# Optimization experiments

Measured on AMD Instinct MI355X. Metric: run time of the kernel, lower is better.

Reference implementation:

```python
import jax, jax.numpy as jnp
import numpy as np

D = 256       # d_model
NH = 8        # heads
K = 7         # neighborhood kernel size
DFF = 1024    # feedforward dim
EPS = 1e-5
B, H, W = 4, 56, 56


def layer_norm(x, g, b):
    m = jnp.mean(x, axis=-1, keepdims=True)
    v = jnp.mean((x - m) ** 2, axis=-1, keepdims=True)
    return (x - m) * jax.lax.rsqrt(v + EPS) * g + b


def neighborhood_attn(x, W_qkv, b_qkv, W_proj, b_proj):
    # NATTEN NeighborhoodAttention2D: each query attends to a KxK window
    # centered on it, clamped (shifted) at borders so every query sees K*K keys.
    Bx, Hx, Wx, C = x.shape
    hd = C // NH
    qkv = x @ W_qkv + b_qkv                      # [B,H,W,3C]
    q, k, v = jnp.split(qkv, 3, axis=-1)
    q = q.reshape(Bx, Hx, Wx, NH, hd)
    k = k.reshape(Bx, Hx, Wx, NH, hd)
    v = v.reshape(Bx, Hx, Wx, NH, hd)
    # neighbor index grids: start = clip(i - K//2, 0, H-K), window = start + [0..K)
    ih = jnp.clip(jnp.arange(Hx) - K // 2, 0, Hx - K)[:, None] + jnp.arange(K)  # [H,K]
    iw = jnp.clip(jnp.arange(Wx) - K // 2, 0, Wx - K)[:, None] + jnp.arange(K)  # [W,K]
    # gather K/V neighborhoods -> [B,H,W,K,K,NH,hd]
    k_nb = k[:, ih[:, None, :, None], iw[None, :, None, :]]
    v_nb = v[:, ih[:, None, :, None], iw[None, :, None, :]]
    attn = jnp.einsum('bhwnd,bhwijnd->bhwnij', q, k_nb) * (hd ** -0.5)
    attn = jax.nn.softmax(attn.reshape(Bx, Hx, Wx, NH, K * K), axis=-1)
    attn = attn.reshape(Bx, Hx, Wx, NH, K, K)
    out = jnp.einsum('bhwnij,bhwijnd->bhwnd', attn, v_nb).reshape(Bx, Hx, Wx, C)
    return out @ W_proj + b_proj


def setup_inputs() -> dict:
    key = jax.random.key(0)
    ks = jax.random.split(key, 8)
    s = 0.02
    return {
        'x': jax.random.normal(ks[0], (B, H, W, D), dtype=jnp.float32),
        'W_qkv': jax.random.normal(ks[1], (D, 3 * D), dtype=jnp.float32) * s,
        'b_qkv': jnp.zeros((3 * D,), dtype=jnp.float32),
        'W_proj': jax.random.normal(ks[2], (D, D), dtype=jnp.float32) * s,
        'b_proj': jnp.zeros((D,), dtype=jnp.float32),
        'W1': jax.random.normal(ks[3], (D, DFF), dtype=jnp.float32) * s,
        'b1': jnp.zeros((DFF,), dtype=jnp.float32),
        'W2': jax.random.normal(ks[4], (DFF, D), dtype=jnp.float32) * s,
        'b2': jnp.zeros((D,), dtype=jnp.float32),
        'g1': jnp.ones((D,), dtype=jnp.float32),
        'be1': jnp.zeros((D,), dtype=jnp.float32),
        'g2': jnp.ones((D,), dtype=jnp.float32),
        'be2': jnp.zeros((D,), dtype=jnp.float32),
    }


def reference(x, W_qkv, b_qkv, W_proj, b_proj, W1, b1, W2, b2, g1, be1, g2, be2):
    # norm_first=False (post-norm): x = norm1(x + mha(x)); x = norm2(x + ff(x))
    a = neighborhood_attn(x, W_qkv, b_qkv, W_proj, b_proj)
    x = layer_norm(x + a, g1, be1)
    f = jax.nn.relu(x @ W1 + b1) @ W2 + b2
    return layer_norm(x + f, g2, be2)
```

## Files before the change

### kernel.cpp

```cpp
#include <hip/hip_runtime.h>
#include <math.h>

#define BATCH 4
#define HH 56
#define WW 56
#define DMODEL 256
#define NHEADS 8
#define HD 32
#define NNB 49
#define NTOK (BATCH*HH*WW)

#define HALO 22
#define NHTOK (HALO*HALO)
#define KV_PAD 40

typedef __attribute__((ext_vector_type(8))) short s16x8;
typedef __attribute__((ext_vector_type(4))) float f32x4;
typedef __attribute__((ext_vector_type(2))) float f32x2;

__device__ inline unsigned short f2b(float f) {
    union { float f; unsigned int u; } v; v.f = f;
    unsigned int r = v.u + 0x7FFF + ((v.u >> 16) & 1);
    return (unsigned short)(r >> 16);
}
__device__ inline float b2f(unsigned short u) {
    union { float f; unsigned int u; } v; v.u = ((unsigned int)u) << 16;
    return v.f;
}

__device__ __forceinline__ f32x2 unpk(unsigned int u) {
    union { unsigned int u; float f; } lo, hi;
    lo.u = u << 16;
    hi.u = u & 0xffff0000u;
    return f32x2{lo.f, hi.f};
}

__device__ __forceinline__ f32x2 pk_fma(f32x2 a, f32x2 b, f32x2 c) {
#if __has_builtin(__builtin_elementwise_fma)
    return __builtin_elementwise_fma(a, b, c);
#else
    return f32x2{fmaf(a.x, b.x, c.x), fmaf(a.y, b.y, c.y)};
#endif
}

__device__ __forceinline__ void async16(const unsigned short* g, unsigned short* l) {
    __builtin_amdgcn_global_load_lds(
        (const __attribute__((address_space(1))) unsigned int*)g,
        (__attribute__((address_space(3))) unsigned int*)l, 16, 0, 0);
}

#define XCAST_BLOCKS 1568
__global__ __launch_bounds__(256)
void prep_kernel(const float* __restrict__ x,
                 const float* __restrict__ Wq, const float* __restrict__ Wp,
                 const float* __restrict__ W1, const float* __restrict__ W2,
                 unsigned short* __restrict__ xb,
                 unsigned short* __restrict__ Wqb, unsigned short* __restrict__ Wpb,
                 unsigned short* __restrict__ W1b, unsigned short* __restrict__ W2b)
{
    if (blockIdx.x < XCAST_BLOCKS) {
        const int i = blockIdx.x * 256 + threadIdx.x;
        const float4* xp = (const float4*)x + (size_t)i * 2;
        const float4 a = xp[0], b = xp[1];
        s16x8 o;
        o[0] = (short)f2b(a.x); o[1] = (short)f2b(a.y);
        o[2] = (short)f2b(a.z); o[3] = (short)f2b(a.w);
        o[4] = (short)f2b(b.x); o[5] = (short)f2b(b.y);
        o[6] = (short)f2b(b.z); o[7] = (short)f2b(b.w);
        *((s16x8*)xb + i) = o;
        return;
    }
    int i = (blockIdx.x - XCAST_BLOCKS) * 256 + threadIdx.x;
    if (i < 196608) {
        int n = i >> 8, k = i & 255;
        Wqb[i] = f2b(Wq[k * 768 + n]);
    } else if ((i -= 196608) < 65536) {
        int n = i >> 8, k = i & 255;
        Wpb[i] = f2b(Wp[k * 256 + n]);
    } else if ((i -= 65536) < 262144) {
        int n = i >> 8, k = i & 255;
        W1b[i] = f2b(W1[k * 1024 + n]);
    } else {
        i -= 262144;
        int n = i >> 10, k = i & 1023;
        W2b[i] = f2b(W2[k * 256 + n]);
    }
}

template<int BN, bool AF32>
__global__ __launch_bounds__(256)
void gemm_k(const unsigned short* __restrict__ Ab, const float* __restrict__ Af,
            const unsigned short* __restrict__ Bt, const float* __restrict__ bias,
            float* __restrict__ outf, unsigned short* __restrict__ outb,
            int M, int N, int K, int relu)
{
    constexpr int NB  = BN / 32;
    constexpr int BPW = BN / 32;
    __shared__ unsigned short As[128 * 64];
    __shared__ unsigned short Bs[BN * 64];

    const int tid = threadIdx.x;
    const int bm = blockIdx.y * 128, bn = blockIdx.x * BN;
    const int wid = tid >> 6, lane = tid & 63;
    const int wm = (wid >> 1) * 64, wn = (wid & 1) * (BN / 2);
    const int row16 = lane & 15, quad = lane >> 4;
    const int crow = lane >> 3, ck8 = (lane & 7) * 8;

    f32x4 acc[4][NB] = {};

    for (int k0 = 0; k0 < K; k0 += 64) {
        float4 fv[8];
        if (AF32) {
            const float* g = Af + (size_t)(bm + (tid >> 1)) * K + k0 + (tid & 1) * 32;
            #pragma unroll
            for (int u = 0; u < 8; ++u) fv[u] = *(const float4*)(g + u * 4);
        }
        __syncthreads();
        if (AF32) {
            unsigned short* d = As + (tid >> 1) * 64 + (tid & 1) * 32;
            #pragma unroll
            for (int u = 0; u < 4; ++u) {
                s16x8 o;
                o[0] = (short)f2b(fv[2*u].x);   o[1] = (short)f2b(fv[2*u].y);
                o[2] = (short)f2b(fv[2*u].z);   o[3] = (short)f2b(fv[2*u].w);
                o[4] = (short)f2b(fv[2*u+1].x); o[5] = (short)f2b(fv[2*u+1].y);
                o[6] = (short)f2b(fv[2*u+1].z); o[7] = (short)f2b(fv[2*u+1].w);
                *(s16x8*)(d + u * 8) = o;
            }
        } else {
            #pragma unroll
            for (int c = 0; c < 4; ++c) {
                const int ch = wid * 4 + c;
                async16(Ab + (size_t)(bm + ch * 8 + crow) * K + k0 + ck8, As + ch * 512);
            }
        }
        #pragma unroll
        for (int c = 0; c < BPW; ++c) {
            const int ch = wid * BPW + c;
            async16(Bt + (size_t)(bn + ch * 8 + crow) * K + k0 + ck8, Bs + ch * 512);
        }
        __syncthreads();

        #pragma unroll
        for (int kc = 0; kc < 2; ++kc) {
            s16x8 af[4], bf[NB];
            #pragma unroll
            for (int i = 0; i < 4; ++i)
                af[i] = *(const s16x8*)(As + (wm + i * 16 + row16) * 64 + kc * 32 + quad * 8);
            #pragma unroll
            for (int j = 0; j < NB; ++j)
                bf[j] = *(const s16x8*)(Bs + (wn + j * 16 + row16) * 64 + kc * 32 + quad * 8);
            #pragma unroll
            for (int i = 0; i < 4; ++i)
                #pragma unroll
                for (int j = 0; j < NB; ++j)
                    acc[i][j] = __builtin_amdgcn_mfma_f32_16x16x32_bf16(af[i], bf[j], acc[i][j], 0, 0, 0);
        }
    }

    #pragma unroll
    for (int j = 0; j < NB; ++j) {
        const int col = bn + wn + j * 16 + row16;
        const float bb = bias[col];
        #pragma unroll
        for (int i = 0; i < 4; ++i) {
            const int r0 = bm + wm + i * 16 + quad * 4;
            #pragma unroll
            for (int reg = 0; reg < 4; ++reg) {
                float v = acc[i][j][reg] + bb;
                if (relu) v = fmaxf(v, 0.f);
                if (outf) outf[(size_t)(r0 + reg) * N + col] = v;
                if (outb) outb[(size_t)(r0 + reg) * N + col] = f2b(v);
            }
        }
    }
}

__global__ __launch_bounds__(256)
void gemm_ln(const unsigned short* __restrict__ Ab, const unsigned short* __restrict__ Bt,
             const float* __restrict__ bias, const float* __restrict__ resid,
             const float* __restrict__ g, const float* __restrict__ beta,
             float* __restrict__ outf, unsigned short* __restrict__ outb, int K)
{
    __shared__ unsigned short As[32 * 64];
    __shared__ unsigned short Bs[256 * 64];

    const int tid = threadIdx.x;
    const int bm = blockIdx.x * 32;
    const int wid = tid >> 6, lane = tid & 63;
    const int wn = wid * 64;
    const int row16 = lane & 15, quad = lane >> 4;
    const int crow = lane >> 3, ck8 = (lane & 7) * 8;

    f32x4 acc[2][4] = {};

    for (int k0 = 0; k0 < K; k0 += 64) {
        __syncthreads();
        #pragma unroll
        for (int c = 0; c < 9; ++c) {
            const int ch = wid * 9 + c;
            if (ch < 4) {
                async16(Ab + (size_t)(bm + ch * 8 + crow) * K + k0 + ck8, As + ch * 512);
            } else {
                const int bc = ch - 4;
                async16(Bt + (size_t)(bc * 8 + crow) * K + k0 + ck8, Bs + bc * 512);
            }
        }
        __syncthreads();

        #pragma unroll
        for (int kc = 0; kc < 2; ++kc) {
            s16x8 af[2], bf[4];
            #pragma unroll
            for (int i = 0; i < 2; ++i)
                af[i] = *(const s16x8*)(As + (i * 16 + row16) * 64 + kc * 32 + quad * 8);
            #pragma unroll
            for (int j = 0; j < 4; ++j)
                bf[j] = *(const s16x8*)(Bs + (wn + j * 16 + row16) * 64 + kc * 32 + quad * 8);
            #pragma unroll
            for (int i = 0; i < 2; ++i)
                #pragma unroll
                for (int j = 0; j < 4; ++j)
                    acc[i][j] = __builtin_amdgcn_mfma_f32_16x16x32_bf16(af[i], bf[j], acc[i][j], 0, 0, 0);
        }
    }

    float bb[4], gv[4], bev[4];
    #pragma unroll
    for (int j = 0; j < 4; ++j) {
        const int col = wn + j * 16 + row16;
        bb[j] = bias[col]; gv[j] = g[col]; bev[j] = beta[col];
    }
    #pragma unroll
    for (int i = 0; i < 2; ++i) {
        #pragma unroll
        for (int reg = 0; reg < 4; ++reg) {
            const size_t rb = (size_t)(bm + i * 16 + quad * 4 + reg) * 256;
            #pragma unroll
            for (int j = 0; j < 4; ++j)
                acc[i][j][reg] += bb[j] + resid[rb + wn + j * 16 + row16];
        }
    }

    __syncthreads();
    float* red = (float*)As;
    #pragma unroll
    for (int i = 0; i < 2; ++i) {
        #pragma unroll
        for (int reg = 0; reg < 4; ++reg) {
            float s1 = 0.f, s2 = 0.f;
            #pragma unroll
            for (int j = 0; j < 4; ++j) {
                const float t = acc[i][j][reg];
                s1 += t; s2 += t * t;
            }
            #pragma unroll
            for (int o = 1; o < 16; o <<= 1) {
                s1 += __shfl_xor(s1, o, 64);
                s2 += __shfl_xor(s2, o, 64);
            }
            if (row16 == 0) {
                const int lrow = i * 16 + quad * 4 + reg;
                red[lrow * 8 + wid * 2]     = s1;
                red[lrow * 8 + wid * 2 + 1] = s2;
            }
        }
    }
    __syncthreads();
    float* stats = red + 256;
    if (tid < 32) {
        const float S1 = red[tid*8] + red[tid*8+2] + red[tid*8+4] + red[tid*8+6];
        const float S2 = red[tid*8+1] + red[tid*8+3] + red[tid*8+5] + red[tid*8+7];
        const float m = S1 * (1.0f / 256.0f);
        const float var = S2 * (1.0f / 256.0f) - m * m;
        stats[tid * 2]     = m;
        stats[tid * 2 + 1] = rsqrtf(var + 1e-5f);
    }
    __syncthreads();

    #pragma unroll
    for (int i = 0; i < 2; ++i) {
        #pragma unroll
        for (int reg = 0; reg < 4; ++reg) {
            const int lrow = i * 16 + quad * 4 + reg;
            const float m = stats[lrow * 2], r = stats[lrow * 2 + 1];
            const size_t rb = (size_t)(bm + lrow) * 256;
            #pragma unroll
            for (int j = 0; j < 4; ++j) {
                const int col = wn + j * 16 + row16;
                const float o = (acc[i][j][reg] - m) * r * gv[j] + bev[j];
                outf[rb + col] = o;
                if (outb) outb[rb + col] = f2b(o);
            }
        }
    }
}

__global__ __launch_bounds__(256, 2)
void natt_kernel(const unsigned short* __restrict__ qkvb, unsigned short* __restrict__ att)
{
    const int blk  = blockIdx.x;
    const int head = blk & 7;
    const int t2   = blk >> 3;
    const int tile = t2 & 15;
    const int b    = t2 >> 4;
    const int r0 = (tile >> 2) * 16, c0 = (tile & 3) * 16;
    const int hs = min(max(r0 - 3, 0), 34);
    const int ws = min(max(c0 - 3, 0), 34);

    __shared__ unsigned short Ks[NHTOK * KV_PAD];
    __shared__ unsigned short Vs[NHTOK * KV_PAD];

    const int tid = threadIdx.x;

    #pragma unroll
    for (int it = 0; it < 8; ++it) {
        const int t = it * 64 + (tid >> 2);
        if (t < NHTOK) {
            const int hr = t / HALO, hc = t - hr * HALO;
            const size_t rb = ((size_t)((b * 56 + hs + hr) * 56 + (ws + hc))) * 768;
            const int d8 = (tid & 3) * 8;
            *(s16x8*)(Ks + t * KV_PAD + d8) = *(const s16x8*)(qkvb + rb + 256 + head * 32 + d8);
            *(s16x8*)(Vs + t * KV_PAD + d8) = *(const s16x8*)(qkvb + rb + 512 + head * 32 + d8);
        }
    }

    const int qh = min(r0 + (tid >> 4), 55);
    const int qw = min(c0 + (tid & 15), 55);
    const int tok = (b * 56 + qh) * 56 + qw;
    const int ro = min(max(qh - 3, 0), 49) - hs;
    const int co = min(max(qw - 3, 0), 49) - ws;

    f32x2 qf[16];
    {
        const unsigned int* qp = (const unsigned int*)(qkvb + (size_t)tok * 768 + head * 32);
        #pragma unroll
        for (int p = 0; p < 16; ++p)
            qf[p] = unpk(qp[p]) * 0.17677669529663687f;
    }
    __syncthreads();

    f32x2 acc[16] = {};
    float sum = 0.f;
    for (int i = 0; i < 7; ++i) {
        const int trow = (ro + i) * HALO + co;
        #pragma unroll
        for (int j = 0; j < 7; ++j) {
            const unsigned int* kp = (const unsigned int*)(Ks + (trow + j) * KV_PAD);
            const unsigned int* vp = (const unsigned int*)(Vs + (trow + j) * KV_PAD);
            const uint4 ka = *(const uint4*)(kp);
            const uint4 kb = *(const uint4*)(kp + 4);
            const uint4 kc = *(const uint4*)(kp + 8);
            const uint4 kd = *(const uint4*)(kp + 12);
            const uint4 va = *(const uint4*)(vp);
            const uint4 vb = *(const uint4*)(vp + 4);
            const uint4 vc = *(const uint4*)(vp + 8);
            const uint4 vd = *(const uint4*)(vp + 12);
            f32x2 sa = {0.f, 0.f}, sb = {0.f, 0.f};
            sa = pk_fma(qf[0],  unpk(ka.x), sa);  sb = pk_fma(qf[1],  unpk(ka.y), sb);
            sa = pk_fma(qf[2],  unpk(ka.z), sa);  sb = pk_fma(qf[3],  unpk(ka.w), sb);
            sa = pk_fma(qf[4],  unpk(kb.x), sa);  sb = pk_fma(qf[5],  unpk(kb.y), sb);
            sa = pk_fma(qf[6],  unpk(kb.z), sa);  sb = pk_fma(qf[7],  unpk(kb.w), sb);
            sa = pk_fma(qf[8],  unpk(kc.x), sa);  sb = pk_fma(qf[9],  unpk(kc.y), sb);
            sa = pk_fma(qf[10], unpk(kc.z), sa);  sb = pk_fma(qf[11], unpk(kc.w), sb);
            sa = pk_fma(qf[12], unpk(kd.x), sa);  sb = pk_fma(qf[13], unpk(kd.y), sb);
            sa = pk_fma(qf[14], unpk(kd.z), sa);  sb = pk_fma(qf[15], unpk(kd.w), sb);
            const float p = __expf(sa.x + sa.y + sb.x + sb.y);
            sum += p;
            const f32x2 pv = {p, p};
            acc[0]  = pk_fma(pv, unpk(va.x), acc[0]);
            acc[1]  = pk_fma(pv, unpk(va.y), acc[1]);
            acc[2]  = pk_fma(pv, unpk(va.z), acc[2]);
            acc[3]  = pk_fma(pv, unpk(va.w), acc[3]);
            acc[4]  = pk_fma(pv, unpk(vb.x), acc[4]);
            acc[5]  = pk_fma(pv, unpk(vb.y), acc[5]);
            acc[6]  = pk_fma(pv, unpk(vb.z), acc[6]);
            acc[7]  = pk_fma(pv, unpk(vb.w), acc[7]);
            acc[8]  = pk_fma(pv, unpk(vc.x), acc[8]);
            acc[9]  = pk_fma(pv, unpk(vc.y), acc[9]);
            acc[10] = pk_fma(pv, unpk(vc.z), acc[10]);
            acc[11] = pk_fma(pv, unpk(vc.w), acc[11]);
            acc[12] = pk_fma(pv, unpk(vd.x), acc[12]);
            acc[13] = pk_fma(pv, unpk(vd.y), acc[13]);
            acc[14] = pk_fma(pv, unpk(vd.z), acc[14]);
            acc[15] = pk_fma(pv, unpk(vd.w), acc[15]);
        }
    }
    const float inv = 1.0f / sum;

    unsigned short* op = att + (size_t)tok * DMODEL + head * 32;
    #pragma unroll
    for (int d4 = 0; d4 < 8; ++d4) {
        ushort4 o;
        o.x = f2b(acc[d4 * 2].x     * inv);
        o.y = f2b(acc[d4 * 2].y     * inv);
        o.z = f2b(acc[d4 * 2 + 1].x * inv);
        o.w = f2b(acc[d4 * 2 + 1].y * inv);
        *(ushort4*)(op + d4 * 4) = o;
    }
}

extern "C" void kernel_launch(void* const* d_in, const int* in_sizes, int n_in,
                              void* d_out, int out_size, void* d_ws, size_t ws_size,
                              hipStream_t stream)
{
    const float* x      = (const float*)d_in[0];
    const float* W_qkv  = (const float*)d_in[1];
    const float* b_qkv  = (const float*)d_in[2];
    const float* W_proj = (const float*)d_in[3];
    const float* b_proj = (const float*)d_in[4];
    const float* W1     = (const float*)d_in[5];
    const float* b1     = (const float*)d_in[6];
    const float* W2     = (const float*)d_in[7];
    const float* b2     = (const float*)d_in[8];
    const float* g1     = (const float*)d_in[9];
    const float* be1    = (const float*)d_in[10];
    const float* g2     = (const float*)d_in[11];
    const float* be2    = (const float*)d_in[12];
    float* out = (float*)d_out;

    char* ws = (char*)d_ws;
    const int M = NTOK;

    unsigned short* qkvb = (unsigned short*)ws;
    unsigned short* h    = (unsigned short*)ws;
    unsigned short* attb = (unsigned short*)(ws + 38535168);
    float*          xn   = (float*)(ws + 57802752);
    unsigned short* xnb  = (unsigned short*)(ws + 70647808);
    unsigned short* Wqb  = (unsigned short*)(ws + 77070336);
    unsigned short* Wpb  = Wqb + 196608;
    unsigned short* W1b  = Wpb + 65536;
    unsigned short* W2b  = W1b + 262144;
    unsigned short* xb   = (unsigned short*)(ws + 78643200);

    dim3 blk(256);

    prep_kernel<<<dim3(XCAST_BLOCKS + 3072), blk, 0, stream>>>(
        x, W_qkv, W_proj, W1, W2, xb, Wqb, Wpb, W1b, W2b);

    gemm_k<128, false><<<dim3(6, 98), blk, 0, stream>>>(xb, nullptr, Wqb, b_qkv, nullptr, qkvb, M, 768, 256, 0);

    natt_kernel<<<dim3(512), blk, 0, stream>>>(qkvb, attb);

    gemm_ln<<<dim3(M / 32), blk, 0, stream>>>(attb, Wpb, b_proj, x, g1, be1, xn, xnb, 256);

    gemm_k<128, false><<<dim3(8, 98), blk, 0, stream>>>(xnb, nullptr, W1b, b1, nullptr, h, M, 1024, 256, 1);

    gemm_ln<<<dim3(M / 32), blk, 0, stream>>>(h, W2b, b2, xn, g2, be2, out, nullptr, 1024);
}
```

Before: 199.6 us.

## Double-buffer LDS tiles in GEMM kernels to overlap loads with MFMA

Both the plain GEMM and the GEMM+LayerNorm kernels now use two shared-memory buffers. The next K-slice is issued with async copies while the current slice is computed, and the barriers per 64-wide K step drop from two to one. This is meant to hide global-load latency behind the matrix instructions. In exchange, shared memory per block doubles, which can lower occupancy. The unused fp32-A path is also removed.

```diff
diff --git a/kernel.cpp b/kernel.cpp
--- a/kernel.cpp
+++ b/kernel.cpp
@@ -87,17 +87,17 @@
     }
 }
 
-template<int BN, bool AF32>
+template<int BN>
 __global__ __launch_bounds__(256)
-void gemm_k(const unsigned short* __restrict__ Ab, const float* __restrict__ Af,
+void gemm_k(const unsigned short* __restrict__ Ab,
             const unsigned short* __restrict__ Bt, const float* __restrict__ bias,
             float* __restrict__ outf, unsigned short* __restrict__ outb,
             int M, int N, int K, int relu)
 {
     constexpr int NB  = BN / 32;
     constexpr int BPW = BN / 32;
-    __shared__ unsigned short As[128 * 64];
-    __shared__ unsigned short Bs[BN * 64];
+    __shared__ unsigned short As[2][128 * 64];
+    __shared__ unsigned short Bs[2][BN * 64];
 
     const int tid = threadIdx.x;
     const int bm = blockIdx.y * 128, bn = blockIdx.x * BN;
@@ -108,54 +108,45 @@
 
     f32x4 acc[4][NB] = {};
 
-    for (int k0 = 0; k0 < K; k0 += 64) {
-        float4 fv[8];
-        if (AF32) {
-            const float* g = Af + (size_t)(bm + (tid >> 1)) * K + k0 + (tid & 1) * 32;
-            #pragma unroll
-            for (int u = 0; u < 8; ++u) fv[u] = *(const float4*)(g + u * 4);
-        }
-        __syncthreads();
-        if (AF32) {
-            unsigned short* d = As + (tid >> 1) * 64 + (tid & 1) * 32;
-            #pragma unroll
-            for (int u = 0; u < 4; ++u) {
-                s16x8 o;
-                o[0] = (short)f2b(fv[2*u].x);   o[1] = (short)f2b(fv[2*u].y);
-                o[2] = (short)f2b(fv[2*u].z);   o[3] = (short)f2b(fv[2*u].w);
-                o[4] = (short)f2b(fv[2*u+1].x); o[5] = (short)f2b(fv[2*u+1].y);
-                o[6] = (short)f2b(fv[2*u+1].z); o[7] = (short)f2b(fv[2*u+1].w);
-                *(s16x8*)(d + u * 8) = o;
-            }
-        } else {
-            #pragma unroll
-            for (int c = 0; c < 4; ++c) {
-                const int ch = wid * 4 + c;
-                async16(Ab + (size_t)(bm + ch * 8 + crow) * K + k0 + ck8, As + ch * 512);
-            }
+    auto stage = [&](int buf, int k0) {
+        #pragma unroll
+        for (int c = 0; c < 4; ++c) {
+            const int ch = wid * 4 + c;
+            async16(Ab + (size_t)(bm + ch * 8 + crow) * K + k0 + ck8, As[buf] + ch * 512);
         }
         #pragma unroll
         for (int c = 0; c < BPW; ++c) {
             const int ch = wid * BPW + c;
-            async16(Bt + (size_t)(bn + ch * 8 + crow) * K + k0 + ck8, Bs + ch * 512);
-        }
-        __syncthreads();
-
+            async16(Bt + (size_t)(bn + ch * 8 + crow) * K + k0 + ck8, Bs[buf] + ch * 512);
+        }
+    };
+    auto compute = [&](int buf) {
         #pragma unroll
         for (int kc = 0; kc < 2; ++kc) {
             s16x8 af[4], bf[NB];
             #pragma unroll
             for (int i = 0; i < 4; ++i)
-                af[i] = *(const s16x8*)(As + (wm + i * 16 + row16) * 64 + kc * 32 + quad * 8);
+                af[i] = *(const s16x8*)(As[buf] + (wm + i * 16 + row16) * 64 + kc * 32 + quad * 8);
             #pragma unroll
             for (int j = 0; j < NB; ++j)
-                bf[j] = *(const s16x8*)(Bs + (wn + j * 16 + row16) * 64 + kc * 32 + quad * 8);
+                bf[j] = *(const s16x8*)(Bs[buf] + (wn + j * 16 + row16) * 64 + kc * 32 + quad * 8);
             #pragma unroll
             for (int i = 0; i < 4; ++i)
                 #pragma unroll
                 for (int j = 0; j < NB; ++j)
                     acc[i][j] = __builtin_amdgcn_mfma_f32_16x16x32_bf16(af[i], bf[j], acc[i][j], 0, 0, 0);
         }
+    };
+
+    stage(0, 0);
+    __syncthreads();
+    for (int k0 = 0; k0 < K; k0 += 128) {
+        stage(1, k0 + 64);
+        compute(0);
+        __syncthreads();
+        if (k0 + 128 < K) stage(0, k0 + 128);
+        compute(1);
+        __syncthreads();
     }
 
     #pragma unroll
@@ -182,8 +173,8 @@
              const float* __restrict__ g, const float* __restrict__ beta,
              float* __restrict__ outf, unsigned short* __restrict__ outb, int K)
 {
-    __shared__ unsigned short As[32 * 64];
-    __shared__ unsigned short Bs[256 * 64];
+    __shared__ unsigned short As[2][32 * 64];
+    __shared__ unsigned short Bs[2][256 * 64];
 
     const int tid = threadIdx.x;
     const int bm = blockIdx.x * 32;
@@ -194,35 +185,45 @@
 
     f32x4 acc[2][4] = {};
 
-    for (int k0 = 0; k0 < K; k0 += 64) {
-        __syncthreads();
+    auto stage = [&](int buf, int k0) {
         #pragma unroll
         for (int c = 0; c < 9; ++c) {
             const int ch = wid * 9 + c;
             if (ch < 4) {
-                async16(Ab + (size_t)(bm + ch * 8 + crow) * K + k0 + ck8, As + ch * 512);
+                async16(Ab + (size_t)(bm + ch * 8 + crow) * K + k0 + ck8, As[buf] + ch * 512);
             } else {
                 const int bc = ch - 4;
-                async16(Bt + (size_t)(bc * 8 + crow) * K + k0 + ck8, Bs + bc * 512);
-            }
-        }
-        __syncthreads();
-
+                async16(Bt + (size_t)(bc * 8 + crow) * K + k0 + ck8, Bs[buf] + bc * 512);
+            }
+        }
+    };
+    auto compute = [&](int buf) {
         #pragma unroll
         for (int kc = 0; kc < 2; ++kc) {
             s16x8 af[2], bf[4];
             #pragma unroll
             for (int i = 0; i < 2; ++i)
-                af[i] = *(const s16x8*)(As + (i * 16 + row16) * 64 + kc * 32 + quad * 8);
+                af[i] = *(const s16x8*)(As[buf] + (i * 16 + row16) * 64 + kc * 32 + quad * 8);
             #pragma unroll
             for (int j = 0; j < 4; ++j)
-                bf[j] = *(const s16x8*)(Bs + (wn + j * 16 + row16) * 64 + kc * 32 + quad * 8);
+                bf[j] = *(const s16x8*)(Bs[buf] + (wn + j * 16 + row16) * 64 + kc * 32 + quad * 8);
             #pragma unroll
             for (int i = 0; i < 2; ++i)
                 #pragma unroll
                 for (int j = 0; j < 4; ++j)
                     acc[i][j] = __builtin_amdgcn_mfma_f32_16x16x32_bf16(af[i], bf[j], acc[i][j], 0, 0, 0);
         }
+    };
+
+    stage(0, 0);
+    __syncthreads();
+    for (int k0 = 0; k0 < K; k0 += 128) {
+        stage(1, k0 + 64);
+        compute(0);
+        __syncthreads();
+        if (k0 + 128 < K) stage(0, k0 + 128);
+        compute(1);
+        __syncthreads();
     }
 
     float bb[4], gv[4], bev[4];
@@ -242,8 +243,7 @@
         }
     }
 
-    __syncthreads();
-    float* red = (float*)As;
+    float* red = (float*)As[0];
     #pragma unroll
     for (int i = 0; i < 2; ++i) {
         #pragma unroll
@@ -438,13 +438,13 @@
     prep_kernel<<<dim3(XCAST_BLOCKS + 3072), blk, 0, stream>>>(
         x, W_qkv, W_proj, W1, W2, xb, Wqb, Wpb, W1b, W2b);
 
-    gemm_k<128, false><<<dim3(6, 98), blk, 0, stream>>>(xb, nullptr, Wqb, b_qkv, nullptr, qkvb, M, 768, 256, 0);
+    gemm_k<128><<<dim3(6, 98), blk, 0, stream>>>(xb, Wqb, b_qkv, nullptr, qkvb, M, 768, 256, 0);
 
     natt_kernel<<<dim3(512), blk, 0, stream>>>(qkvb, attb);
 
     gemm_ln<<<dim3(M / 32), blk, 0, stream>>>(attb, Wpb, b_proj, x, g1, be1, xn, xnb, 256);
 
-    gemm_k<128, false><<<dim3(8, 98), blk, 0, stream>>>(xnb, nullptr, W1b, b1, nullptr, h, M, 1024, 256, 1);
+    gemm_k<128><<<dim3(8, 98), blk, 0, stream>>>(xnb, W1b, b1, nullptr, h, M, 1024, 256, 1);
 
     gemm_ln<<<dim3(M / 32), blk, 0, stream>>>(h, W2b, b2, xn, g2, be2, out, nullptr, 1024);
 }
```

Result: no change. 199.2 us (-0.2%).
